# Kernel optimization log

Hardware: AMD Instinct MI355X
Metric: run time of the kernel (lower is better)

## Reference

```python
import jax, jax.numpy as jnp
import numpy as np

B, S, D = 32, 576, 1024  # [batch*num_windows^2, window_len, hidden]
H = 16
HD = D // H
DFF = 4 * D
EPS = 1e-6


def _layernorm(x, g, b):
    mu = jnp.mean(x, axis=-1, keepdims=True)
    var = jnp.mean(jnp.square(x - mu), axis=-1, keepdims=True)
    return (x - mu) * jax.lax.rsqrt(var + EPS) * g + b


def setup_inputs() -> dict:
    key = jax.random.key(0)
    ks = jax.random.split(key, 12)
    s_d = 1.0 / np.sqrt(D)
    s_ff = 1.0 / np.sqrt(DFF)
    return {
        "hidden_states": jax.random.normal(ks[0], (B, S, D), jnp.float32),
        "norm1_g": jnp.ones((D,), jnp.float32),
        "norm1_b": jnp.zeros((D,), jnp.float32),
        "wq": jax.random.normal(ks[1], (D, D), jnp.float32) * s_d,
        "bq": jnp.zeros((D,), jnp.float32),
        "wk": jax.random.normal(ks[2], (D, D), jnp.float32) * s_d,
        "bk": jnp.zeros((D,), jnp.float32),
        "wv": jax.random.normal(ks[3], (D, D), jnp.float32) * s_d,
        "bv": jnp.zeros((D,), jnp.float32),
        "wo": jax.random.normal(ks[4], (D, D), jnp.float32) * s_d,
        "bo": jnp.zeros((D,), jnp.float32),
        "ls1": jnp.ones((D,), jnp.float32),
        "norm2_g": jnp.ones((D,), jnp.float32),
        "norm2_b": jnp.zeros((D,), jnp.float32),
        "w1": jax.random.normal(ks[5], (D, DFF), jnp.float32) * s_d,
        "b1": jnp.zeros((DFF,), jnp.float32),
        "w2": jax.random.normal(ks[6], (DFF, D), jnp.float32) * s_ff,
        "b2": jnp.zeros((D,), jnp.float32),
        "ls2": jnp.ones((D,), jnp.float32),
    }


def reference(hidden_states, norm1_g, norm1_b, wq, bq, wk, bk, wv, bv, wo, bo,
              ls1, norm2_g, norm2_b, w1, b1, w2, b2, ls2):
    x = hidden_states
    shortcut = x
    xn = _layernorm(x, norm1_g, norm1_b)
    # separate Q/K/V projections, per-window attention (windows folded into batch)
    q = (xn @ wq + bq).reshape(B, S, H, HD)
    k = (xn @ wk + bk).reshape(B, S, H, HD)
    v = (xn @ wv + bv).reshape(B, S, H, HD)
    scale = jnp.asarray(HD, q.dtype) ** -0.5
    scores = jnp.einsum("bqhd,bkhd->bhqk", q, k) * scale
    attn = jax.nn.softmax(scores, axis=-1)
    ctx = jnp.einsum("bhqk,bkhd->bqhd", attn, v).reshape(B, S, D)
    attn_out = (ctx @ wo + bo) * ls1  # LayerScale 1; DropPath identity at inference
    x = attn_out + shortcut
    yn = _layernorm(x, norm2_g, norm2_b)
    h = jax.nn.gelu(yn @ w1 + b1, approximate=False)
    mlp_out = (h @ w2 + b2) * ls2
    return mlp_out + x
```

## Files before the change

kernel.cpp:

```cpp
#include <hip/hip_runtime.h>
#include <hip/hip_bf16.h>
#include <math.h>


typedef __attribute__((ext_vector_type(8))) short bf16x8;
typedef __attribute__((ext_vector_type(4))) float f32x4;

static constexpr int S_LEN = 576;
static constexpr int D_DIM = 1024;
static constexpr int M_ROWS = 32 * 576;

__device__ __forceinline__ unsigned short f2bf(float f) {
  unsigned u = __builtin_bit_cast(unsigned, f);
  u += 0x7FFFu + ((u >> 16) & 1u);
  return (unsigned short)(u >> 16);
}

__device__ __forceinline__ f32x4 mfma16(bf16x8 a, bf16x8 b, f32x4 c) {
  return __builtin_amdgcn_mfma_f32_16x16x32_bf16(a, b, c, 0, 0, 0);
}

__device__ __forceinline__ void gload_lds16(const void* g, void* l) {
  __builtin_amdgcn_global_load_lds(
      (const __attribute__((address_space(1))) unsigned int*)g,
      (__attribute__((address_space(3))) unsigned int*)l, 16, 0, 0);
}

__global__ __launch_bounds__(256) void transpose_cast_kernel(
    const float* __restrict__ in, unsigned short* __restrict__ out, int R, int C) {
  __shared__ float tile[32][33];
  const int bx = blockIdx.x * 32;
  const int by = blockIdx.y * 32;
  const int tx = threadIdx.x & 31, ty = threadIdx.x >> 5;
#pragma unroll
  for (int i = 0; i < 4; ++i) {
    int r = ty + i * 8;
    tile[r][tx] = in[(size_t)(by + r) * C + bx + tx];
  }
  __syncthreads();
#pragma unroll
  for (int i = 0; i < 4; ++i) {
    int r = ty + i * 8;
    out[(size_t)(bx + r) * R + by + tx] = f2bf(tile[tx][r]);
  }
}

__global__ __launch_bounds__(256) void ln_kernel(
    const float* __restrict__ x, const float* __restrict__ g,
    const float* __restrict__ bta, unsigned short* __restrict__ out) {
  const int row = blockIdx.x;
  const int t = threadIdx.x;
  const float* xr = x + (size_t)row * D_DIM;
  float4 v = *(const float4*)&xr[t * 4];
  float s = v.x + v.y + v.z + v.w;
  float sq = v.x * v.x + v.y * v.y + v.z * v.z + v.w * v.w;
#pragma unroll
  for (int o = 32; o; o >>= 1) {
    s += __shfl_xor(s, o);
    sq += __shfl_xor(sq, o);
  }
  __shared__ float sa[4], sb[4];
  const int wid = t >> 6, lane = t & 63;
  if (lane == 0) { sa[wid] = s; sb[wid] = sq; }
  __syncthreads();
  s = sa[0] + sa[1] + sa[2] + sa[3];
  sq = sb[0] + sb[1] + sb[2] + sb[3];
  const float mu = s * (1.0f / D_DIM);
  const float var = sq * (1.0f / D_DIM) - mu * mu;
  const float rstd = rsqrtf(var + 1e-6f);
  float4 gv = *(const float4*)&g[t * 4];
  float4 bv = *(const float4*)&bta[t * 4];
  ushort4 o4;
  o4.x = f2bf((v.x - mu) * rstd * gv.x + bv.x);
  o4.y = f2bf((v.y - mu) * rstd * gv.y + bv.y);
  o4.z = f2bf((v.z - mu) * rstd * gv.z + bv.z);
  o4.w = f2bf((v.w - mu) * rstd * gv.w + bv.w);
  *(ushort4*)&out[(size_t)row * D_DIM + t * 4] = o4;
}

enum { EPI_BF16_BIAS = 0, EPI_F32_RES = 1, EPI_GELU = 2 };

template <int EPI>
__global__ __launch_bounds__(256) void gemm_bt(
    const unsigned short* __restrict__ A, const unsigned short* __restrict__ Bt,
    int K, int N, const float* __restrict__ bias, const float* __restrict__ ls,
    const float* __restrict__ res, unsigned short* __restrict__ outb,
    float* __restrict__ outf) {
  __shared__ __align__(16) unsigned short Al[128 * 32];
  __shared__ __align__(16) unsigned short Bl[128 * 32];
  const int m0 = blockIdx.y * 128, n0 = blockIdx.x * 128;
  const int tid = threadIdx.x, lane = tid & 63, wid = tid >> 6;
  const int wm = wid >> 1, wn = wid & 1;
  const int l15 = lane & 15, lg = lane >> 4;
  const int srow = lane >> 2;
  const int scol = (lane & 3) * 8;

  f32x4 acc[4][4];
#pragma unroll
  for (int m = 0; m < 4; ++m)
#pragma unroll
    for (int n = 0; n < 4; ++n) acc[m][n] = (f32x4)0.0f;

  for (int k0 = 0; k0 < K; k0 += 32) {
#pragma unroll
    for (int c = 0; c < 2; ++c) {
      const int r = wid * 32 + c * 16;
      gload_lds16(A + (size_t)(m0 + r + srow) * K + k0 + scol, &Al[r * 32]);
      gload_lds16(Bt + (size_t)(n0 + r + srow) * K + k0 + scol, &Bl[r * 32]);
    }
    __syncthreads();
    bf16x8 af[4], bfr[4];
#pragma unroll
    for (int m = 0; m < 4; ++m)
      af[m] = *(const bf16x8*)&Al[(wm * 64 + m * 16 + l15) * 32 + lg * 8];
#pragma unroll
    for (int n = 0; n < 4; ++n)
      bfr[n] = *(const bf16x8*)&Bl[(wn * 64 + n * 16 + l15) * 32 + lg * 8];
#pragma unroll
    for (int m = 0; m < 4; ++m)
#pragma unroll
      for (int n = 0; n < 4; ++n) acc[m][n] = mfma16(af[m], bfr[n], acc[m][n]);
    __syncthreads();
  }

#pragma unroll
  for (int m = 0; m < 4; ++m) {
    const int rowb = m0 + wm * 64 + m * 16 + lg * 4;
#pragma unroll
    for (int n = 0; n < 4; ++n) {
      const int col = n0 + wn * 64 + n * 16 + l15;
      const float bcol = bias[col];
#pragma unroll
      for (int r = 0; r < 4; ++r) {
        const int grow = rowb + r;
        const float vacc = acc[m][n][r] + bcol;
        if constexpr (EPI == EPI_BF16_BIAS) {
          outb[(size_t)grow * N + col] = f2bf(vacc);
        } else if constexpr (EPI == EPI_GELU) {
          const float gv = 0.5f * vacc * (1.0f + erff(vacc * 0.70710678118654752f));
          outb[(size_t)grow * N + col] = f2bf(gv);
        } else {
          outf[(size_t)grow * N + col] =
              vacc * ls[col] + res[(size_t)grow * N + col];
        }
      }
    }
  }
}

__global__ __launch_bounds__(256) void attn_kernel(
    const unsigned short* __restrict__ q, const unsigned short* __restrict__ k,
    const unsigned short* __restrict__ v, unsigned short* __restrict__ ctx) {
  __shared__ __align__(16) unsigned short Vt[64][40];
  __shared__ __align__(16) unsigned short P[4][16][40];
  const int bh = blockIdx.y, b = bh >> 4, h = bh & 15;
  const int q0 = blockIdx.x * 64;
  const int tid = threadIdx.x, lane = tid & 63, wid = tid >> 6;
  const int l15 = lane & 15, lg = lane >> 4;
  const size_t base = (size_t)b * S_LEN * D_DIM + h * 64;

  const int qrow = q0 + wid * 16 + l15;
  const bf16x8 qf0 = *(const bf16x8*)(q + base + (size_t)qrow * D_DIM + lg * 8);
  const bf16x8 qf1 = *(const bf16x8*)(q + base + (size_t)qrow * D_DIM + 32 + lg * 8);

  f32x4 acc_o[4];
#pragma unroll
  for (int nt = 0; nt < 4; ++nt) acc_o[nt] = (f32x4)0.0f;
  float mrow[4] = {-3e38f, -3e38f, -3e38f, -3e38f};
  float lrow[4] = {0.f, 0.f, 0.f, 0.f};

  const int vkey = tid >> 3, vchunk = tid & 7;

  for (int kt = 0; kt < S_LEN / 32; ++kt) {
    __syncthreads();
    {
      const bf16x8 vv = *(const bf16x8*)(v + base + (size_t)(kt * 32 + vkey) * D_DIM + vchunk * 8);
#pragma unroll
      for (int j = 0; j < 8; ++j) Vt[vchunk * 8 + j][vkey] = (unsigned short)vv[j];
    }
    f32x4 s0 = (f32x4)0.0f, s1 = (f32x4)0.0f;
    {
      const size_t kr0 = base + (size_t)(kt * 32 + l15) * D_DIM;
      const size_t kr1 = base + (size_t)(kt * 32 + 16 + l15) * D_DIM;
      bf16x8 k00 = *(const bf16x8*)(k + kr0 + lg * 8);
      bf16x8 k01 = *(const bf16x8*)(k + kr0 + 32 + lg * 8);
      bf16x8 k10 = *(const bf16x8*)(k + kr1 + lg * 8);
      bf16x8 k11 = *(const bf16x8*)(k + kr1 + 32 + lg * 8);
      s0 = mfma16(qf0, k00, s0);
      s0 = mfma16(qf1, k01, s0);
      s1 = mfma16(qf0, k10, s1);
      s1 = mfma16(qf1, k11, s1);
    }
    __syncthreads();
    float al[4];
#pragma unroll
    for (int r = 0; r < 4; ++r) {
      const float x0 = s0[r] * 0.125f, x1 = s1[r] * 0.125f;
      float mt = fmaxf(x0, x1);
      mt = fmaxf(mt, __shfl_xor(mt, 1));
      mt = fmaxf(mt, __shfl_xor(mt, 2));
      mt = fmaxf(mt, __shfl_xor(mt, 4));
      mt = fmaxf(mt, __shfl_xor(mt, 8));
      const float mn = fmaxf(mrow[r], mt);
      const float a = __expf(mrow[r] - mn);
      const float p0 = __expf(x0 - mn), p1 = __expf(x1 - mn);
      float rs = p0 + p1;
      rs += __shfl_xor(rs, 1);
      rs += __shfl_xor(rs, 2);
      rs += __shfl_xor(rs, 4);
      rs += __shfl_xor(rs, 8);
      lrow[r] = lrow[r] * a + rs;
      mrow[r] = mn;
      al[r] = a;
      P[wid][lg * 4 + r][l15] = f2bf(p0);
      P[wid][lg * 4 + r][l15 + 16] = f2bf(p1);
    }
#pragma unroll
    for (int nt = 0; nt < 4; ++nt) {
      f32x4 t = acc_o[nt];
      t[0] *= al[0]; t[1] *= al[1]; t[2] *= al[2]; t[3] *= al[3];
      acc_o[nt] = t;
    }
    const bf16x8 pf = *(const bf16x8*)&P[wid][l15][lg * 8];
#pragma unroll
    for (int nt = 0; nt < 4; ++nt) {
      const bf16x8 vf = *(const bf16x8*)&Vt[nt * 16 + l15][lg * 8];
      acc_o[nt] = mfma16(pf, vf, acc_o[nt]);
    }
  }
#pragma unroll
  for (int nt = 0; nt < 4; ++nt) {
#pragma unroll
    for (int r = 0; r < 4; ++r) {
      const int grow = q0 + wid * 16 + lg * 4 + r;
      ctx[base + (size_t)grow * D_DIM + nt * 16 + l15] =
          f2bf(acc_o[nt][r] / lrow[r]);
    }
  }
}

extern "C" void kernel_launch(void* const* d_in, const int* in_sizes, int n_in,
                              void* d_out, int out_size, void* d_ws, size_t ws_size,
                              hipStream_t stream) {
  const float* x   = (const float*)d_in[0];
  const float* n1g = (const float*)d_in[1];
  const float* n1b = (const float*)d_in[2];
  const float* wq  = (const float*)d_in[3];
  const float* bq  = (const float*)d_in[4];
  const float* wk  = (const float*)d_in[5];
  const float* bk  = (const float*)d_in[6];
  const float* wv  = (const float*)d_in[7];
  const float* bv  = (const float*)d_in[8];
  const float* wo  = (const float*)d_in[9];
  const float* bo  = (const float*)d_in[10];
  const float* ls1 = (const float*)d_in[11];
  const float* n2g = (const float*)d_in[12];
  const float* n2b = (const float*)d_in[13];
  const float* w1  = (const float*)d_in[14];
  const float* b1  = (const float*)d_in[15];
  const float* w2  = (const float*)d_in[16];
  const float* b2  = (const float*)d_in[17];
  const float* ls2 = (const float*)d_in[18];
  float* out = (float*)d_out;

  char* ws = (char*)d_ws;
  const size_t MB = 1ull << 20;
  unsigned short* wqt = (unsigned short*)(ws + 0 * MB);
  unsigned short* wkt = (unsigned short*)(ws + 2 * MB);
  unsigned short* wvt = (unsigned short*)(ws + 4 * MB);
  unsigned short* wot = (unsigned short*)(ws + 6 * MB);
  unsigned short* w1t = (unsigned short*)(ws + 8 * MB);
  unsigned short* w2t = (unsigned short*)(ws + 16 * MB);
  unsigned short* xn  = (unsigned short*)(ws + 24 * MB);
  unsigned short* qb  = (unsigned short*)(ws + 60 * MB);
  unsigned short* kb  = (unsigned short*)(ws + 96 * MB);
  unsigned short* vb  = (unsigned short*)(ws + 132 * MB);
  unsigned short* ctx = xn;
  unsigned short* hbuf = xn;
  unsigned short* yn  = (unsigned short*)(ws + 168 * MB);
  (void)ws_size; (void)in_sizes; (void)n_in; (void)out_size;

  const dim3 blk(256);
  transpose_cast_kernel<<<dim3(32, 32), blk, 0, stream>>>(wq, wqt, 1024, 1024);
  transpose_cast_kernel<<<dim3(32, 32), blk, 0, stream>>>(wk, wkt, 1024, 1024);
  transpose_cast_kernel<<<dim3(32, 32), blk, 0, stream>>>(wv, wvt, 1024, 1024);
  transpose_cast_kernel<<<dim3(32, 32), blk, 0, stream>>>(wo, wot, 1024, 1024);
  transpose_cast_kernel<<<dim3(128, 32), blk, 0, stream>>>(w1, w1t, 1024, 4096);
  transpose_cast_kernel<<<dim3(32, 128), blk, 0, stream>>>(w2, w2t, 4096, 1024);
  ln_kernel<<<dim3(M_ROWS), blk, 0, stream>>>(x, n1g, n1b, xn);
  gemm_bt<EPI_BF16_BIAS><<<dim3(8, 144), blk, 0, stream>>>(
      xn, wqt, 1024, 1024, bq, nullptr, nullptr, qb, nullptr);
  gemm_bt<EPI_BF16_BIAS><<<dim3(8, 144), blk, 0, stream>>>(
      xn, wkt, 1024, 1024, bk, nullptr, nullptr, kb, nullptr);
  gemm_bt<EPI_BF16_BIAS><<<dim3(8, 144), blk, 0, stream>>>(
      xn, wvt, 1024, 1024, bv, nullptr, nullptr, vb, nullptr);
  attn_kernel<<<dim3(9, 512), blk, 0, stream>>>(qb, kb, vb, ctx);
  gemm_bt<EPI_F32_RES><<<dim3(8, 144), blk, 0, stream>>>(
      ctx, wot, 1024, 1024, bo, ls1, x, nullptr, out);
  ln_kernel<<<dim3(M_ROWS), blk, 0, stream>>>(out, n2g, n2b, yn);
  gemm_bt<EPI_GELU><<<dim3(32, 144), blk, 0, stream>>>(
      yn, w1t, 1024, 4096, b1, nullptr, nullptr, hbuf, nullptr);
  gemm_bt<EPI_F32_RES><<<dim3(8, 144), blk, 0, stream>>>(
      hbuf, w2t, 4096, 1024, b2, ls2, out, nullptr, out);
}
```

Before: 1.317 ms.

## Replace GEMMs with 256x256 double-buffered swizzled kernel and fuse QKV projection

Replaces the 128x128 single-stage GEMM with a 256x256 tile, 512-thread kernel using double-buffered LDS with XOR swizzle, phased prefetch with explicit waitcnt/barriers, and XCD-aware block remapping. The three Q/K/V projections are fused into one GEMM over a concatenated weight and bias, and attention reads the interleaved QKV buffer. Larger tiles raise arithmetic intensity and overlap loads with MFMA, at the cost of heavy LDS use and register pressure that limit occupancy.

```diff
diff --git a/kernel.cpp b/kernel.cpp
--- a/kernel.cpp
+++ b/kernel.cpp
@@ -8,7 +8,7 @@
 
 static constexpr int S_LEN = 576;
 static constexpr int D_DIM = 1024;
-static constexpr int M_ROWS = 32 * 576;
+static constexpr int M_ROWS = 18432;
 
 __device__ __forceinline__ unsigned short f2bf(float f) {
   unsigned u = __builtin_bit_cast(unsigned, f);
@@ -29,8 +29,7 @@
 __global__ __launch_bounds__(256) void transpose_cast_kernel(
     const float* __restrict__ in, unsigned short* __restrict__ out, int R, int C) {
   __shared__ float tile[32][33];
-  const int bx = blockIdx.x * 32;
-  const int by = blockIdx.y * 32;
+  const int bx = blockIdx.x * 32, by = blockIdx.y * 32;
   const int tx = threadIdx.x & 31, ty = threadIdx.x >> 5;
 #pragma unroll
   for (int i = 0; i < 4; ++i) {
@@ -43,6 +42,13 @@
     int r = ty + i * 8;
     out[(size_t)(bx + r) * R + by + tx] = f2bf(tile[tx][r]);
   }
+}
+
+__global__ __launch_bounds__(256) void concat3_kernel(
+    const float* __restrict__ a, const float* __restrict__ b,
+    const float* __restrict__ c, float* __restrict__ o) {
+  int i = blockIdx.x * 256 + threadIdx.x;
+  o[i] = (i < 1024) ? a[i] : (i < 2048 ? b[i - 1024] : c[i - 2048]);
 }
 
 __global__ __launch_bounds__(256) void ln_kernel(
@@ -80,64 +86,126 @@
 
 enum { EPI_BF16_BIAS = 0, EPI_F32_RES = 1, EPI_GELU = 2 };
 
+#define VM4 asm volatile("s_waitcnt vmcnt(4)" ::: "memory");
+#define VM0 asm volatile("s_waitcnt vmcnt(0)" ::: "memory");
+
+#define STAGE(GPTR, BASE, LDK, KT, H, LDSBASE)                                \
+  if ((KT) < NT) {                                                            \
+    const int rb_ = (H) * 128 + wid * 16;                                     \
+    gload_lds16((GPTR) + (size_t)((BASE) + rb_ + rlo) * (LDK) +               \
+                    (size_t)(KT) * 64 + slsw * 8,                             \
+                (LDSBASE) + rb_ * 64);                                        \
+    gload_lds16((GPTR) + (size_t)((BASE) + rb_ + 8 + rlo) * (LDK) +           \
+                    (size_t)(KT) * 64 + slsw * 8,                             \
+                (LDSBASE) + (rb_ + 8) * 64);                                  \
+  }
+
+#define PHASE(AP, BP, Q, VMSTMT, ...)                                         \
+  {                                                                           \
+    _Pragma("unroll") for (int mm = 0; mm < 2; ++mm)                          \
+      _Pragma("unroll") for (int ks = 0; ks < 2; ++ks)                        \
+        af[mm][ks] = *(const bf16x8*)((AP) + (2 * (Q) + mm) * 1024 +          \
+                                      (((ks * 4 + lg) ^ l7) * 8));            \
+    if ((Q) == 0) {                                                           \
+      _Pragma("unroll") for (int n = 0; n < 4; ++n)                           \
+        _Pragma("unroll") for (int ks = 0; ks < 2; ++ks)                      \
+          bfr[n][ks] = *(const bf16x8*)((BP) + n * 1024 +                     \
+                                        (((ks * 4 + lg) ^ l7) * 8));          \
+    }                                                                         \
+    __VA_ARGS__;                                                              \
+    __builtin_amdgcn_s_barrier();                                             \
+    asm volatile("s_waitcnt lgkmcnt(0)" ::: "memory");                        \
+    __builtin_amdgcn_sched_barrier(0);                                        \
+    __builtin_amdgcn_s_setprio(1);                                            \
+    _Pragma("unroll") for (int mm = 0; mm < 2; ++mm)                          \
+      _Pragma("unroll") for (int n = 0; n < 4; ++n) {                         \
+        acc[2 * (Q) + mm][n] = mfma16(af[mm][0], bfr[n][0], acc[2*(Q)+mm][n]);\
+        acc[2 * (Q) + mm][n] = mfma16(af[mm][1], bfr[n][1], acc[2*(Q)+mm][n]);\
+      }                                                                       \
+    __builtin_amdgcn_s_setprio(0);                                            \
+    VMSTMT;                                                                   \
+    __builtin_amdgcn_s_barrier();                                             \
+  }
+
 template <int EPI>
-__global__ __launch_bounds__(256) void gemm_bt(
+__global__ __launch_bounds__(512, 2) void gemm256(
     const unsigned short* __restrict__ A, const unsigned short* __restrict__ Bt,
-    int K, int N, const float* __restrict__ bias, const float* __restrict__ ls,
+    const int K, const int N, const int NN,
+    const float* __restrict__ bias, const float* __restrict__ ls,
     const float* __restrict__ res, unsigned short* __restrict__ outb,
     float* __restrict__ outf) {
-  __shared__ __align__(16) unsigned short Al[128 * 32];
-  __shared__ __align__(16) unsigned short Bl[128 * 32];
-  const int m0 = blockIdx.y * 128, n0 = blockIdx.x * 128;
+  __shared__ __align__(16) unsigned short As[2][256 * 64];
+  __shared__ __align__(16) unsigned short Bs[2][256 * 64];
+
+  const int nwg = gridDim.x;
+  const int orig = blockIdx.x;
+  const int q8 = nwg >> 3, r8 = nwg & 7;
+  const int xcd = orig & 7, lid = orig >> 3;
+  const int swz =
+      (xcd < r8 ? xcd * (q8 + 1) : r8 * (q8 + 1) + (xcd - r8) * q8) + lid;
+  const int m0 = (swz / NN) * 256, n0 = (swz % NN) * 256;
+
   const int tid = threadIdx.x, lane = tid & 63, wid = tid >> 6;
-  const int wm = wid >> 1, wn = wid & 1;
-  const int l15 = lane & 15, lg = lane >> 4;
-  const int srow = lane >> 2;
-  const int scol = (lane & 3) * 8;
-
-  f32x4 acc[4][4];
-#pragma unroll
-  for (int m = 0; m < 4; ++m)
+  const int wm = wid >> 2, wn = wid & 3;
+  const int l15 = lane & 15, lg = lane >> 4, l7 = lane & 7;
+  const int rlo = lane >> 3;
+  const int slsw = (lane & 7) ^ rlo;
+
+  const unsigned short* Ap0 = &As[0][0] + (wm * 128 + l15) * 64;
+  const unsigned short* Ap1 = &As[1][0] + (wm * 128 + l15) * 64;
+  const unsigned short* Bp0 = &Bs[0][0] + (wn * 64 + l15) * 64;
+  const unsigned short* Bp1 = &Bs[1][0] + (wn * 64 + l15) * 64;
+
+  const int NT = K >> 6;
+
+  f32x4 acc[8][4];
+#pragma unroll
+  for (int m = 0; m < 8; ++m)
 #pragma unroll
     for (int n = 0; n < 4; ++n) acc[m][n] = (f32x4)0.0f;
-
-  for (int k0 = 0; k0 < K; k0 += 32) {
-#pragma unroll
-    for (int c = 0; c < 2; ++c) {
-      const int r = wid * 32 + c * 16;
-      gload_lds16(A + (size_t)(m0 + r + srow) * K + k0 + scol, &Al[r * 32]);
-      gload_lds16(Bt + (size_t)(n0 + r + srow) * K + k0 + scol, &Bl[r * 32]);
-    }
-    __syncthreads();
-    bf16x8 af[4], bfr[4];
-#pragma unroll
-    for (int m = 0; m < 4; ++m)
-      af[m] = *(const bf16x8*)&Al[(wm * 64 + m * 16 + l15) * 32 + lg * 8];
-#pragma unroll
-    for (int n = 0; n < 4; ++n)
-      bfr[n] = *(const bf16x8*)&Bl[(wn * 64 + n * 16 + l15) * 32 + lg * 8];
-#pragma unroll
-    for (int m = 0; m < 4; ++m)
-#pragma unroll
-      for (int n = 0; n < 4; ++n) acc[m][n] = mfma16(af[m], bfr[n], acc[m][n]);
-    __syncthreads();
-  }
-
-#pragma unroll
-  for (int m = 0; m < 4; ++m) {
-    const int rowb = m0 + wm * 64 + m * 16 + lg * 4;
+  bf16x8 af[2][2], bfr[4][2];
+
+  STAGE(A, m0, K, 0, 0, &As[0][0]);
+  STAGE(A, m0, K, 0, 1, &As[0][0]);
+  STAGE(Bt, n0, K, 0, 0, &Bs[0][0]);
+  STAGE(Bt, n0, K, 0, 1, &Bs[0][0]);
+  STAGE(Bt, n0, K, 1, 0, &Bs[1][0]);
+  STAGE(Bt, n0, K, 1, 1, &Bs[1][0]);
+  VM4;
+  __builtin_amdgcn_s_barrier();
+
+  const int NIT = NT >> 1;
+  for (int it = 0; it < NIT; ++it) {
+    const int T = it * 2;
+    const bool last = (it == NIT - 1);
+    PHASE(Ap0, Bp0, 0, , STAGE(A, m0, K, T + 1, 0, &As[1][0]))
+    PHASE(Ap0, Bp0, 1, , STAGE(A, m0, K, T + 1, 1, &As[1][0]))
+    PHASE(Ap0, Bp0, 2, , STAGE(Bt, n0, K, T + 2, 0, &Bs[0][0]))
+    PHASE(Ap0, Bp0, 3, if (last) { VM0 } else { VM4 },
+          STAGE(Bt, n0, K, T + 2, 1, &Bs[0][0]))
+    PHASE(Ap1, Bp1, 0, , STAGE(A, m0, K, T + 2, 0, &As[0][0]))
+    PHASE(Ap1, Bp1, 1, , STAGE(A, m0, K, T + 2, 1, &As[0][0]))
+    PHASE(Ap1, Bp1, 2, , STAGE(Bt, n0, K, T + 3, 0, &Bs[1][0]))
+    PHASE(Ap1, Bp1, 3, VM4, STAGE(Bt, n0, K, T + 3, 1, &Bs[1][0]))
+  }
+
+  const int rowbase = m0 + wm * 128 + lg * 4;
+  const int colbase = n0 + wn * 64 + l15;
+#pragma unroll
+  for (int m = 0; m < 8; ++m) {
 #pragma unroll
     for (int n = 0; n < 4; ++n) {
-      const int col = n0 + wn * 64 + n * 16 + l15;
+      const int col = colbase + n * 16;
       const float bcol = bias[col];
 #pragma unroll
       for (int r = 0; r < 4; ++r) {
-        const int grow = rowb + r;
+        const int grow = rowbase + m * 16 + r;
         const float vacc = acc[m][n][r] + bcol;
         if constexpr (EPI == EPI_BF16_BIAS) {
           outb[(size_t)grow * N + col] = f2bf(vacc);
         } else if constexpr (EPI == EPI_GELU) {
-          const float gv = 0.5f * vacc * (1.0f + erff(vacc * 0.70710678118654752f));
+          const float gv =
+              0.5f * vacc * (1.0f + erff(vacc * 0.70710678118654752f));
           outb[(size_t)grow * N + col] = f2bf(gv);
         } else {
           outf[(size_t)grow * N + col] =
@@ -149,19 +217,21 @@
 }
 
 __global__ __launch_bounds__(256) void attn_kernel(
-    const unsigned short* __restrict__ q, const unsigned short* __restrict__ k,
-    const unsigned short* __restrict__ v, unsigned short* __restrict__ ctx) {
+    const unsigned short* __restrict__ qkv, unsigned short* __restrict__ ctx) {
   __shared__ __align__(16) unsigned short Vt[64][40];
   __shared__ __align__(16) unsigned short P[4][16][40];
   const int bh = blockIdx.y, b = bh >> 4, h = bh & 15;
   const int q0 = blockIdx.x * 64;
   const int tid = threadIdx.x, lane = tid & 63, wid = tid >> 6;
   const int l15 = lane & 15, lg = lane >> 4;
-  const size_t base = (size_t)b * S_LEN * D_DIM + h * 64;
+  const size_t base = (size_t)b * S_LEN * 3072 + h * 64;
+  const unsigned short* q = qkv + base;
+  const unsigned short* k = qkv + base + 1024;
+  const unsigned short* v = qkv + base + 2048;
 
   const int qrow = q0 + wid * 16 + l15;
-  const bf16x8 qf0 = *(const bf16x8*)(q + base + (size_t)qrow * D_DIM + lg * 8);
-  const bf16x8 qf1 = *(const bf16x8*)(q + base + (size_t)qrow * D_DIM + 32 + lg * 8);
+  const bf16x8 qf0 = *(const bf16x8*)(q + (size_t)qrow * 3072 + lg * 8);
+  const bf16x8 qf1 = *(const bf16x8*)(q + (size_t)qrow * 3072 + 32 + lg * 8);
 
   f32x4 acc_o[4];
 #pragma unroll
@@ -174,14 +244,15 @@
   for (int kt = 0; kt < S_LEN / 32; ++kt) {
     __syncthreads();
     {
-      const bf16x8 vv = *(const bf16x8*)(v + base + (size_t)(kt * 32 + vkey) * D_DIM + vchunk * 8);
+      const bf16x8 vv =
+          *(const bf16x8*)(v + (size_t)(kt * 32 + vkey) * 3072 + vchunk * 8);
 #pragma unroll
       for (int j = 0; j < 8; ++j) Vt[vchunk * 8 + j][vkey] = (unsigned short)vv[j];
     }
     f32x4 s0 = (f32x4)0.0f, s1 = (f32x4)0.0f;
     {
-      const size_t kr0 = base + (size_t)(kt * 32 + l15) * D_DIM;
-      const size_t kr1 = base + (size_t)(kt * 32 + 16 + l15) * D_DIM;
+      const size_t kr0 = (size_t)(kt * 32 + l15) * 3072;
+      const size_t kr1 = (size_t)(kt * 32 + 16 + l15) * 3072;
       bf16x8 k00 = *(const bf16x8*)(k + kr0 + lg * 8);
       bf16x8 k01 = *(const bf16x8*)(k + kr0 + 32 + lg * 8);
       bf16x8 k10 = *(const bf16x8*)(k + kr1 + lg * 8);
@@ -233,7 +304,7 @@
 #pragma unroll
     for (int r = 0; r < 4; ++r) {
       const int grow = q0 + wid * 16 + lg * 4 + r;
-      ctx[base + (size_t)grow * D_DIM + nt * 16 + l15] =
+      ctx[(size_t)(b * S_LEN + grow) * 1024 + h * 64 + nt * 16 + l15] =
           f2bf(acc_o[nt][r] / lrow[r]);
     }
   }
@@ -264,42 +335,35 @@
   float* out = (float*)d_out;
 
   char* ws = (char*)d_ws;
-  const size_t MB = 1ull << 20;
-  unsigned short* wqt = (unsigned short*)(ws + 0 * MB);
-  unsigned short* wkt = (unsigned short*)(ws + 2 * MB);
-  unsigned short* wvt = (unsigned short*)(ws + 4 * MB);
-  unsigned short* wot = (unsigned short*)(ws + 6 * MB);
-  unsigned short* w1t = (unsigned short*)(ws + 8 * MB);
-  unsigned short* w2t = (unsigned short*)(ws + 16 * MB);
-  unsigned short* xn  = (unsigned short*)(ws + 24 * MB);
-  unsigned short* qb  = (unsigned short*)(ws + 60 * MB);
-  unsigned short* kb  = (unsigned short*)(ws + 96 * MB);
-  unsigned short* vb  = (unsigned short*)(ws + 132 * MB);
-  unsigned short* ctx = xn;
-  unsigned short* hbuf = xn;
-  unsigned short* yn  = (unsigned short*)(ws + 168 * MB);
+  unsigned short* wqkvt = (unsigned short*)(ws + 0);
+  unsigned short* wot   = (unsigned short*)(ws + 6291456);
+  unsigned short* w1t   = (unsigned short*)(ws + 8388608);
+  unsigned short* w2t   = (unsigned short*)(ws + 16777216);
+  unsigned short* xn    = (unsigned short*)(ws + 25165824);
+  unsigned short* qkvb  = (unsigned short*)(ws + 62914560);
+  unsigned short* yn    = (unsigned short*)(ws + 176160768);
+  float*          bqkv  = (float*)(ws + 176160768);
+  unsigned short* ctx   = xn;
+  unsigned short* hbuf  = xn;
   (void)ws_size; (void)in_sizes; (void)n_in; (void)out_size;
 
   const dim3 blk(256);
-  transpose_cast_kernel<<<dim3(32, 32), blk, 0, stream>>>(wq, wqt, 1024, 1024);
-  transpose_cast_kernel<<<dim3(32, 32), blk, 0, stream>>>(wk, wkt, 1024, 1024);
-  transpose_cast_kernel<<<dim3(32, 32), blk, 0, stream>>>(wv, wvt, 1024, 1024);
+  concat3_kernel<<<dim3(12), blk, 0, stream>>>(bq, bk, bv, bqkv);
+  transpose_cast_kernel<<<dim3(32, 32), blk, 0, stream>>>(wq, wqkvt, 1024, 1024);
+  transpose_cast_kernel<<<dim3(32, 32), blk, 0, stream>>>(wk, wqkvt + 1024 * 1024, 1024, 1024);
+  transpose_cast_kernel<<<dim3(32, 32), blk, 0, stream>>>(wv, wqkvt + 2048 * 1024, 1024, 1024);
   transpose_cast_kernel<<<dim3(32, 32), blk, 0, stream>>>(wo, wot, 1024, 1024);
   transpose_cast_kernel<<<dim3(128, 32), blk, 0, stream>>>(w1, w1t, 1024, 4096);
   transpose_cast_kernel<<<dim3(32, 128), blk, 0, stream>>>(w2, w2t, 4096, 1024);
   ln_kernel<<<dim3(M_ROWS), blk, 0, stream>>>(x, n1g, n1b, xn);
-  gemm_bt<EPI_BF16_BIAS><<<dim3(8, 144), blk, 0, stream>>>(
-      xn, wqt, 1024, 1024, bq, nullptr, nullptr, qb, nullptr);
-  gemm_bt<EPI_BF16_BIAS><<<dim3(8, 144), blk, 0, stream>>>(
-      xn, wkt, 1024, 1024, bk, nullptr, nullptr, kb, nullptr);
-  gemm_bt<EPI_BF16_BIAS><<<dim3(8, 144), blk, 0, stream>>>(
-      xn, wvt, 1024, 1024, bv, nullptr, nullptr, vb, nullptr);
-  attn_kernel<<<dim3(9, 512), blk, 0, stream>>>(qb, kb, vb, ctx);
-  gemm_bt<EPI_F32_RES><<<dim3(8, 144), blk, 0, stream>>>(
-      ctx, wot, 1024, 1024, bo, ls1, x, nullptr, out);
+  gemm256<EPI_BF16_BIAS><<<dim3(72 * 12), dim3(512), 0, stream>>>(
+      xn, wqkvt, 1024, 3072, 12, bqkv, nullptr, nullptr, qkvb, nullptr);
+  attn_kernel<<<dim3(9, 512), blk, 0, stream>>>(qkvb, ctx);
+  gemm256<EPI_F32_RES><<<dim3(72 * 4), dim3(512), 0, stream>>>(
+      ctx, wot, 1024, 1024, 4, bo, ls1, x, nullptr, out);
   ln_kernel<<<dim3(M_ROWS), blk, 0, stream>>>(out, n2g, n2b, yn);
-  gemm_bt<EPI_GELU><<<dim3(32, 144), blk, 0, stream>>>(
-      yn, w1t, 1024, 4096, b1, nullptr, nullptr, hbuf, nullptr);
-  gemm_bt<EPI_F32_RES><<<dim3(8, 144), blk, 0, stream>>>(
-      hbuf, w2t, 4096, 1024, b2, ls2, out, nullptr, out);
-}
+  gemm256<EPI_GELU><<<dim3(72 * 16), dim3(512), 0, stream>>>(
+      yn, w1t, 1024, 4096, 16, b1, nullptr, nullptr, hbuf, nullptr);
+  gemm256<EPI_F32_RES><<<dim3(72 * 4), dim3(512), 0, stream>>>(
+      hbuf, w2t, 4096, 1024, 4, b2, ls2, out, nullptr, out);
+}
```

New measurement: 1.154 ms. -12.4%, faster.
